# Performance work log

Hardware: AMD Instinct MI355X
Metric: run time of the kernel (lower is better)

## Reference

```python
import jax, jax.numpy as jnp
import numpy as np

NUM_BUCKETS = 32
MAX_DISTANCE = 128
NUM_HEADS = 16
D_KV = 64


def _relative_position_bucket(relative_position):
    # bidirectional buckets, faithful to T5Attention._relative_position_bucket
    num_buckets = NUM_BUCKETS // 2
    relative_buckets = (relative_position > 0).astype(jnp.int32) * num_buckets
    relative_position = jnp.abs(relative_position)
    max_exact = num_buckets // 2
    is_small = relative_position < max_exact
    rp_f = relative_position.astype(jnp.float32)
    rel_if_large = max_exact + (
        jnp.log(rp_f / max_exact) / np.log(MAX_DISTANCE / max_exact) * (num_buckets - max_exact)
    )
    rel_if_large = jnp.minimum(rel_if_large, num_buckets - 1)
    relative_buckets = relative_buckets + jnp.where(is_small, rp_f, rel_if_large).astype(jnp.int32)
    return relative_buckets


def setup_inputs() -> dict:
    key = jax.random.key(0)
    ks = jax.random.split(key, 6)
    B, S, D = 2, 2048, 1024
    inner = NUM_HEADS * D_KV  # 1024
    q_std = (inner * D_KV) ** (-0.5)
    kv_std = inner ** (-0.5)
    return {
        "hidden_states": jax.random.normal(ks[0], (B, S, D), jnp.float32),
        "attention_mask": jnp.ones((B, S), jnp.int32),
        "Wq": jax.random.normal(ks[1], (D, inner), jnp.float32) * q_std,
        "Wk": jax.random.normal(ks[2], (D, inner), jnp.float32) * kv_std,
        "Wv": jax.random.normal(ks[3], (D, inner), jnp.float32) * kv_std,
        "Wo": jax.random.normal(ks[4], (inner, D), jnp.float32) * kv_std,
        "rel_bias": jax.random.normal(ks[5], (NUM_BUCKETS, NUM_HEADS), jnp.float32),
    }


def reference(hidden_states, attention_mask, Wq, Wk, Wv, Wo, rel_bias):
    B, S, D = hidden_states.shape
    H, Dk = NUM_HEADS, D_KV

    q = (hidden_states @ Wq).reshape(B, S, H, Dk)
    k = (hidden_states @ Wk).reshape(B, S, H, Dk)
    v = (hidden_states @ Wv).reshape(B, S, H, Dk)
    q = q / jnp.sqrt(jnp.asarray(Dk, q.dtype))

    scores = jnp.einsum('bthd,bshd->bhts', q, k)  # [B,H,S,S]

    # relative position bias
    pos = jnp.arange(S, dtype=jnp.int32)
    rel_pos = pos[None, :] - pos[:, None]          # memory - context, [S,S]
    buckets = _relative_position_bucket(rel_pos)   # [S,S]
    bias = rel_bias[buckets]                       # [S,S,H]
    scores = scores + bias.transpose(2, 0, 1)[None].astype(scores.dtype)

    mask = attention_mask[:, None, None, :].astype(scores.dtype)
    scores = scores + (1.0 - mask) * jnp.finfo(scores.dtype).min

    attn = jax.nn.softmax(scores, axis=-1)
    out = jnp.einsum('bhts,bshd->bthd', attn, v).reshape(B, S, H * Dk)
    return out @ Wo
```

## Files before the change

kernel.cpp:

```cpp
#include <hip/hip_runtime.h>
#include <hip/hip_bf16.h>
#include <math.h>

typedef __attribute__((ext_vector_type(8))) short bf16x8;
typedef __attribute__((ext_vector_type(4))) short s16x4;
typedef __attribute__((ext_vector_type(4))) float f32x4;

constexpr int cB = 2, cS = 2048, cH = 16, cD = 64, cIn = 1024, cM = 1024;
constexpr float cLog2e = 1.4426950408889634f;

union BfPack { bf16x8 v; short s[8]; };
union BfPack4 { s16x4 v; short s[4]; };

__device__ __forceinline__ short f2bf(float f) {
    union { float f; unsigned u; } v; v.f = f;
    unsigned r = v.u + 0x7fffu + ((v.u >> 16) & 1u);
    return (short)(r >> 16);
}

__device__ __forceinline__ f32x4 mfma16(bf16x8 a, bf16x8 b, f32x4 c) {
    return __builtin_amdgcn_mfma_f32_16x16x32_bf16(a, b, c, 0, 0, 0);
}

__device__ __forceinline__ void async16(const short* g, short* l) {
    __builtin_amdgcn_global_load_lds(
        (const __attribute__((address_space(1))) unsigned*)(uintptr_t)g,
        (__attribute__((address_space(3))) unsigned*)(uintptr_t)l, 16, 0, 0);
}

__global__ __launch_bounds__(256) void prep_kernel(
    const float* __restrict__ hidden, short* __restrict__ hbf,
    const float* __restrict__ Wq, const float* __restrict__ Wk,
    const float* __restrict__ Wv, const float* __restrict__ Wo,
    short* __restrict__ Wt,
    const float* __restrict__ rel_bias, const int* __restrict__ mask,
    float* __restrict__ bt, float* __restrict__ maskadd) {
    const int bid = blockIdx.x;
    const int tid = threadIdx.x;
    if (bid < 2048) {
        int t = bid * 256 + tid;
        const float4* src = (const float4*)hidden;
        float4 a = src[2 * t], b = src[2 * t + 1];
        BfPack p;
        p.s[0] = f2bf(a.x); p.s[1] = f2bf(a.y); p.s[2] = f2bf(a.z); p.s[3] = f2bf(a.w);
        p.s[4] = f2bf(b.x); p.s[5] = f2bf(b.y); p.s[6] = f2bf(b.z); p.s[7] = f2bf(b.w);
        ((bf16x8*)hbf)[t] = p.v;
    } else if (bid < 3072) {
        const int b2 = bid - 2048;
        const int z = b2 >> 8, rem = b2 & 255;
        const float* W = (z == 0) ? Wq : (z == 1) ? Wk : (z == 2) ? Wv : Wo;
        const float scale = (z == 0) ? 0.125f * cLog2e : 1.0f;
        const int n0 = (rem & 15) * 64, k0 = (rem >> 4) * 64;
        __shared__ short sW[64][72];
        const int r = tid >> 2, c4 = (tid & 3) * 16;
        {
            const float* src = W + (size_t)(k0 + r) * cM + n0 + c4;
            BfPack p[2];
            #pragma unroll
            for (int q = 0; q < 2; q++) {
                float4 x = ((const float4*)src)[2 * q];
                float4 y = ((const float4*)src)[2 * q + 1];
                p[q].s[0] = f2bf(x.x * scale); p[q].s[1] = f2bf(x.y * scale);
                p[q].s[2] = f2bf(x.z * scale); p[q].s[3] = f2bf(x.w * scale);
                p[q].s[4] = f2bf(y.x * scale); p[q].s[5] = f2bf(y.y * scale);
                p[q].s[6] = f2bf(y.z * scale); p[q].s[7] = f2bf(y.w * scale);
            }
            *(bf16x8*)&sW[r][c4] = p[0].v;
            *(bf16x8*)&sW[r][c4 + 8] = p[1].v;
        }
        __syncthreads();
        const int n = tid >> 2, kc = (tid & 3) * 16;
        BfPack o0, o1;
        #pragma unroll
        for (int j = 0; j < 8; j++) o0.s[j] = sW[kc + j][n];
        #pragma unroll
        for (int j = 0; j < 8; j++) o1.s[j] = sW[kc + 8 + j][n];
        short* dst = Wt + (size_t)z * cM * cIn + (size_t)(n0 + n) * cIn + k0 + kc;
        *(bf16x8*)dst = o0.v;
        *(bf16x8*)(dst + 8) = o1.v;
    } else {
        int idx = (bid - 3072) * 256 + tid;
        if (idx < 4096) maskadd[idx] = (1.0f - (float)mask[idx]) * -3.0e38f;
        if (idx >= 4095) return;
        int delta = idx - 2047;
        int rb = (delta > 0) ? 16 : 0;
        int ar = delta < 0 ? -delta : delta;
        int bucket;
        if (ar < 8) {
            bucket = rb + ar;
        } else {
            float rl = 8.0f + logf((float)ar * 0.125f) * 2.8853900817779268f;
            rl = fminf(rl, 15.0f);
            bucket = rb + (int)rl;
        }
        #pragma unroll
        for (int h = 0; h < cH; h++)
            bt[h * 4096 + 2048 + delta] = rel_bias[bucket * cH + h] * cLog2e;
    }
}

template <bool SWAP>
__device__ __forceinline__ void gemm_core(
    const short* __restrict__ A, const short* __restrict__ Bt,
    short* smem, int m0, int c0, int tid, f32x4 (&acc)[4][4]) {
    short* sA = smem;
    short* sB = smem + 4096;
    const int w = tid >> 6, l = tid & 63;
    const int m16 = l & 15, g = l >> 4;
    const int srow = l >> 2, scol = (l & 3) * 8;
    const int mq = (w & 1) * 64, nq = (w >> 1) * 64;

    for (int k0 = 0; k0 < cIn; k0 += 32) {
        __syncthreads();
        async16(A + (size_t)(m0 + w * 16 + srow) * cIn + k0 + scol,
                sA + w * 512 + l * 8);
        async16(A + (size_t)(m0 + 64 + w * 16 + srow) * cIn + k0 + scol,
                sA + 2048 + w * 512 + l * 8);
        async16(Bt + (size_t)(c0 + w * 16 + srow) * cIn + k0 + scol,
                sB + w * 512 + l * 8);
        async16(Bt + (size_t)(c0 + 64 + w * 16 + srow) * cIn + k0 + scol,
                sB + 2048 + w * 512 + l * 8);
        __syncthreads();
        bf16x8 af[4], bf[4];
        #pragma unroll
        for (int i = 0; i < 4; i++)
            af[i] = *(const bf16x8*)(sA + (mq + i * 16 + m16) * 32 + g * 8);
        #pragma unroll
        for (int j = 0; j < 4; j++)
            bf[j] = *(const bf16x8*)(sB + (nq + j * 16 + m16) * 32 + g * 8);
        #pragma unroll
        for (int i = 0; i < 4; i++)
            #pragma unroll
            for (int j = 0; j < 4; j++)
                acc[i][j] = SWAP ? mfma16(bf[j], af[i], acc[i][j])
                                 : mfma16(af[i], bf[j], acc[i][j]);
    }
}

__global__ __launch_bounds__(256) void gemm_qkv_kernel(
    const short* __restrict__ hbf, const short* __restrict__ Wt,
    short* __restrict__ Qrm, short* __restrict__ Krm, short* __restrict__ VT) {
    const int z = blockIdx.z;
    const short* Bt = Wt + (size_t)z * cM * cIn;
    const int m0 = blockIdx.y * 128, c0 = blockIdx.x * 128;
    __shared__ short smem[128 * 132];
    const int tid = threadIdx.x, w = tid >> 6, l = tid & 63;
    const int m16 = l & 15, g = l >> 4;
    const int mq = (w & 1) * 64, nq = (w >> 1) * 64;
    f32x4 acc[4][4] = {};

    if (z <= 1) {
        gemm_core<false>(hbf, Bt, smem, m0, c0, tid, acc);
        __syncthreads();
        #pragma unroll
        for (int i = 0; i < 4; i++)
            #pragma unroll
            for (int j = 0; j < 4; j++)
                #pragma unroll
                for (int r = 0; r < 4; r++)
                    smem[(mq + i * 16 + g * 4 + r) * 132 + nq + j * 16 + m16] =
                        f2bf(acc[i][j][r]);
        __syncthreads();
        const int tr = tid >> 1, hf = (tid & 1) * 64;
        short* dst = ((z == 0) ? Qrm : Krm) + (size_t)(m0 + tr) * cM + c0 + hf;
        #pragma unroll
        for (int c = 0; c < 8; c++)
            *(bf16x8*)(dst + c * 8) = *(const bf16x8*)(smem + tr * 132 + hf + c * 8);
    } else {
        gemm_core<true>(hbf, Bt, smem, m0, c0, tid, acc);
        __syncthreads();
        #pragma unroll
        for (int i = 0; i < 4; i++) {
            const int sl = mq + i * 16 + m16;
            const int s6 = sl & 63;
            const int pcol = (sl & 64) +
                             ((s6 & 3) | ((s6 & 28) << 1) | ((s6 >> 3) & 4));
            #pragma unroll
            for (int j = 0; j < 4; j++)
                #pragma unroll
                for (int r = 0; r < 4; r++)
                    smem[(nq + j * 16 + g * 4 + r) * 132 + pcol] =
                        f2bf(acc[i][j][r]);
        }
        __syncthreads();
        const int tr = tid >> 1, hf = (tid & 1) * 64;
        const int wcol = c0 + tr;
        short* dst = VT + (((size_t)(m0 >> 11) * cH + (wcol >> 6)) * cD +
                           (wcol & 63)) * cS + (m0 & 2047) + hf;
        #pragma unroll
        for (int c = 0; c < 8; c++)
            *(bf16x8*)(dst + c * 8) = *(const bf16x8*)(smem + tr * 132 + hf + c * 8);
    }
}

__global__ __launch_bounds__(256, 2) void attn_kernel(
    const short* __restrict__ Qrm, const short* __restrict__ Krm,
    const short* __restrict__ VTK, const float* __restrict__ maskadd,
    const float* __restrict__ bias_t, short* __restrict__ ctx) {
    const int raw = blockIdx.x;
    const int xcd = raw & 7, j = raw >> 3;
    const int qi = j & 15, grp = j >> 4;
    const int bh = grp * 8 + xcd;
    const int b = bh >> 4, h = bh & 15;
    const int q0 = qi * 128;

    const short* VTp = VTK + ((size_t)b * cH + h) * cS * cD;
    const float* bh_ = bias_t + h * 4096 + 2048;
    const float* mp = maskadd + b * cS;

    const int tid = threadIdx.x;
    const int wave = tid >> 6, lane = tid & 63;
    const int m16 = lane & 15, g = lane >> 4;

    __shared__ short Kt[2][128 * 64];
    __shared__ short Vt[2][64 * 128];

    int qv[2];
    bf16x8 qf[2][2];
    #pragma unroll
    for (int qq = 0; qq < 2; qq++) {
        qv[qq] = q0 + qq * 64 + wave * 16 + m16;
        const short* qb = Qrm + (size_t)(b * cS + qv[qq]) * cM + h * cD;
        qf[qq][0] = *(const bf16x8*)(qb + g * 8);
        qf[qq][1] = *(const bf16x8*)(qb + 32 + g * 8);
    }

    f32x4 o[2][4] = {};
    f32x4 lacc[2] = {};
    BfPack ones;
    #pragma unroll
    for (int i = 0; i < 8; i++) ones.s[i] = (short)0x3F80;

    const int u8 = tid & 7, r8 = tid >> 3;
    const int u16s = tid & 15, r16 = tid >> 4;
    const short* pK = Krm + ((size_t)b * cS + r8) * cM + h * cD +
                      ((u8 ^ (r8 & 7)) << 3);
    const short* pV = VTp + (size_t)r16 * cS + ((u16s ^ (r16 & 7)) << 3);
    short* dK = (short*)Kt + tid * 8;
    short* dV = (short*)Vt + tid * 8;

    const int kx0 = ((g ^ (m16 & 7)) << 3);
    const int kx1 = (((g + 4) ^ (m16 & 7)) << 3);

    #pragma unroll
    for (int c = 0; c < 4; c++) {
        async16(pK + (size_t)(c * 32) * cM, dK + c * 2048);
        async16(pV + (size_t)(c * 16) * cS, dV + c * 2048);
    }
    __syncthreads();

    for (int kt = 0; kt < cS; kt += 128) {
        const int buf = (kt >> 7) & 1, nxt = buf ^ 1;
        if (kt + 128 < cS) {
            #pragma unroll
            for (int c = 0; c < 4; c++) {
                async16(pK + (size_t)(kt + 128 + c * 32) * cM,
                        dK + nxt * 8192 + c * 2048);
                async16(pV + (size_t)(c * 16) * cS + kt + 128,
                        dV + nxt * 8192 + c * 2048);
            }
        }
        const short* K_ = (const short*)Kt + buf * 8192;
        const short* V_ = (const short*)Vt + buf * 8192;

        #pragma unroll
        for (int h2 = 0; h2 < 2; h2++) {
            f32x4 binit[2][4];
            #pragma unroll
            for (int t4 = 0; t4 < 4; t4++) {
                const int keyb = kt + (h2 * 4 + t4) * 16 + g * 4;
                #pragma unroll
                for (int qq = 0; qq < 2; qq++)
                    #pragma unroll
                    for (int c = 0; c < 4; c++)
                        binit[qq][t4][c] = bh_[keyb + c - qv[qq]] + mp[keyb + c];
            }

            f32x4 s[2][4];
            __builtin_amdgcn_s_setprio(1);
            #pragma unroll
            for (int t4 = 0; t4 < 4; t4++) {
                const int st = h2 * 4 + t4;
                bf16x8 klo = *(const bf16x8*)(K_ + (st * 16 + m16) * 64 + kx0);
                bf16x8 khi = *(const bf16x8*)(K_ + (st * 16 + m16) * 64 + kx1);
                #pragma unroll
                for (int qq = 0; qq < 2; qq++) {
                    f32x4 z4 = {};
                    s[qq][t4] = mfma16(khi, qf[qq][1],
                                       mfma16(klo, qf[qq][0], z4));
                }
            }
            __builtin_amdgcn_s_setprio(0);

            BfPack pp[2][2];
            #pragma unroll
            for (int qq = 0; qq < 2; qq++)
                #pragma unroll
                for (int t4 = 0; t4 < 4; t4++)
                    #pragma unroll
                    for (int r = 0; r < 2; r++) {
                        float p0 = __builtin_amdgcn_exp2f(s[qq][t4][2 * r] +
                                                          binit[qq][t4][2 * r]);
                        float p1 = __builtin_amdgcn_exp2f(s[qq][t4][2 * r + 1] +
                                                          binit[qq][t4][2 * r + 1]);
                        __hip_bfloat162 h2v = __float22bfloat162_rn(float2{p0, p1});
                        short2 sp = *(short2*)&h2v;
                        pp[qq][t4 & 1].s[(t4 >> 1) * 4 + 2 * r]     = sp.x;
                        pp[qq][t4 & 1].s[(t4 >> 1) * 4 + 2 * r + 1] = sp.y;
                    }

            __builtin_amdgcn_s_setprio(1);
            #pragma unroll
            for (int qq = 0; qq < 2; qq++) {
                lacc[qq] = mfma16(ones.v, pp[qq][0].v, lacc[qq]);
                lacc[qq] = mfma16(ones.v, pp[qq][1].v, lacc[qq]);
            }
            #pragma unroll
            for (int nt = 0; nt < 4; nt++) {
                bf16x8 vlo = *(const bf16x8*)(V_ + (nt * 16 + m16) * 128 +
                                              h2 * 64 + kx0);
                bf16x8 vhi = *(const bf16x8*)(V_ + (nt * 16 + m16) * 128 +
                                              h2 * 64 + kx1);
                #pragma unroll
                for (int qq = 0; qq < 2; qq++) {
                    o[qq][nt] = mfma16(vlo, pp[qq][0].v, o[qq][nt]);
                    o[qq][nt] = mfma16(vhi, pp[qq][1].v, o[qq][nt]);
                }
            }
            __builtin_amdgcn_s_setprio(0);
        }

        __syncthreads();
    }

    #pragma unroll
    for (int qq = 0; qq < 2; qq++) {
        const float inv = 1.0f / lacc[qq][0];
        short* cb = ctx + (size_t)(b * cS + qv[qq]) * cM + h * cD;
        #pragma unroll
        for (int nt = 0; nt < 4; nt++) {
            BfPack4 pk;
            #pragma unroll
            for (int r = 0; r < 4; r++) pk.s[r] = f2bf(o[qq][nt][r] * inv);
            *(s16x4*)(cb + nt * 16 + g * 4) = pk.v;
        }
    }
}

__global__ __launch_bounds__(256) void gemm_o_kernel(
    const short* __restrict__ ctx, const short* __restrict__ WoT,
    float* __restrict__ out) {
    const int m0 = blockIdx.y * 64, c0 = blockIdx.x * 128;
    __shared__ short smem[6144];
    short* sA = smem;
    short* sB = smem + 2048;
    const int tid = threadIdx.x, w = tid >> 6, l = tid & 63;
    const int m16 = l & 15, g = l >> 4;
    const int wm = (w & 1) * 32, wn = (w >> 1) * 64;
    const int sr = tid >> 2, sc = (tid & 3) * 8;
    f32x4 acc[2][4] = {};

    for (int k0 = 0; k0 < cIn; k0 += 32) {
        __syncthreads();
        async16(ctx + (size_t)(m0 + (sr & 63)) * cIn + k0 + sc, sA + tid * 8);
        async16(WoT + (size_t)(c0 + sr) * cIn + k0 + sc, sB + tid * 8);
        async16(WoT + (size_t)(c0 + 64 + sr) * cIn + k0 + sc, sB + 2048 + tid * 8);
        __syncthreads();
        bf16x8 af[2], bf[4];
        #pragma unroll
        for (int i = 0; i < 2; i++)
            af[i] = *(const bf16x8*)(sA + (wm + i * 16 + m16) * 32 + g * 8);
        #pragma unroll
        for (int jj = 0; jj < 4; jj++)
            bf[jj] = *(const bf16x8*)(sB + (wn + jj * 16 + m16) * 32 + g * 8);
        #pragma unroll
        for (int i = 0; i < 2; i++)
            #pragma unroll
            for (int jj = 0; jj < 4; jj++)
                acc[i][jj] = mfma16(af[i], bf[jj], acc[i][jj]);
    }
    #pragma unroll
    for (int i = 0; i < 2; i++)
        #pragma unroll
        for (int jj = 0; jj < 4; jj++)
            #pragma unroll
            for (int r = 0; r < 4; r++)
                out[(size_t)(m0 + wm + i * 16 + g * 4 + r) * cM +
                    c0 + wn + jj * 16 + m16] = acc[i][jj][r];
}

extern "C" void kernel_launch(void* const* d_in, const int* in_sizes, int n_in,
                              void* d_out, int out_size, void* d_ws, size_t ws_size,
                              hipStream_t stream) {
    const float* hidden   = (const float*)d_in[0];
    const int*   mask     = (const int*)d_in[1];
    const float* Wq       = (const float*)d_in[2];
    const float* Wk       = (const float*)d_in[3];
    const float* Wv       = (const float*)d_in[4];
    const float* Wo       = (const float*)d_in[5];
    const float* rel_bias = (const float*)d_in[6];
    float* out = (float*)d_out;

    short* hbf_ctx = (short*)d_ws;
    short* Wt  = hbf_ctx + (size_t)4 * 1024 * 1024;
    short* Qrm = Wt  + (size_t)4 * 1024 * 1024;
    short* Krm = Qrm + (size_t)4 * 1024 * 1024;
    short* VT  = Krm + (size_t)4 * 1024 * 1024;
    float* bias_t  = (float*)(VT + (size_t)4 * 1024 * 1024);
    float* maskf   = bias_t + 16 * 4096;

    prep_kernel<<<3088, 256, 0, stream>>>(hidden, hbf_ctx, Wq, Wk, Wv, Wo, Wt,
                                          rel_bias, mask, bias_t, maskf);
    gemm_qkv_kernel<<<dim3(8, 32, 3), 256, 0, stream>>>(hbf_ctx, Wt, Qrm, Krm, VT);
    attn_kernel<<<512, 256, 0, stream>>>(Qrm, Krm, VT, maskf, bias_t, hbf_ctx);
    gemm_o_kernel<<<dim3(8, 64), 256, 0, stream>>>(hbf_ctx, Wt + (size_t)3 * 1024 * 1024,
                                                   out);
}
```

Measured before the change: 197.1 us.

## Load V directly from global into registers and vectorize bias loads via phase-shifted tables

The attention kernel stops staging V tiles through shared memory and instead loads V fragments straight from global memory into registers each half-tile. The relative-position bias table is expanded into four phase-shifted copies, so each lane can read its four bias values as one aligned float4; the mask add is likewise read as a float4. This cuts LDS traffic and footprint and replaces scalar gathers with vector loads, at the cost of uncached global V reads on the critical path and a four-times-larger bias table written in prep.

```diff
diff --git a/kernel.cpp b/kernel.cpp
--- a/kernel.cpp
+++ b/kernel.cpp
@@ -80,22 +80,26 @@
         *(bf16x8*)(dst + 8) = o1.v;
     } else {
         int idx = (bid - 3072) * 256 + tid;
-        if (idx < 4096) maskadd[idx] = (1.0f - (float)mask[idx]) * -3.0e38f;
-        if (idx >= 4095) return;
-        int delta = idx - 2047;
-        int rb = (delta > 0) ? 16 : 0;
-        int ar = delta < 0 ? -delta : delta;
-        int bucket;
-        if (ar < 8) {
-            bucket = rb + ar;
-        } else {
-            float rl = 8.0f + logf((float)ar * 0.125f) * 2.8853900817779268f;
-            rl = fminf(rl, 15.0f);
-            bucket = rb + (int)rl;
-        }
-        #pragma unroll
-        for (int h = 0; h < cH; h++)
-            bt[h * 4096 + 2048 + delta] = rel_bias[bucket * cH + h] * cLog2e;
+        maskadd[idx] = (1.0f - (float)mask[idx]) * -3.0e38f;
+        #pragma unroll
+        for (int p = 0; p < 4; p++) {
+            int delta = idx - 2048 + p;
+            if (delta > 2047) delta = 2047;
+            int rb = (delta > 0) ? 16 : 0;
+            int ar = delta < 0 ? -delta : delta;
+            int bucket;
+            if (ar < 8) {
+                bucket = rb + ar;
+            } else {
+                float rl = 8.0f + logf((float)ar * 0.125f) * 2.8853900817779268f;
+                rl = fminf(rl, 15.0f);
+                bucket = rb + (int)rl;
+            }
+            #pragma unroll
+            for (int h = 0; h < cH; h++)
+                bt[((size_t)(p * cH + h)) * 4096 + idx] =
+                    rel_bias[bucket * cH + h] * cLog2e;
+        }
     }
 }
 
@@ -196,7 +200,7 @@
 __global__ __launch_bounds__(256, 2) void attn_kernel(
     const short* __restrict__ Qrm, const short* __restrict__ Krm,
     const short* __restrict__ VTK, const float* __restrict__ maskadd,
-    const float* __restrict__ bias_t, short* __restrict__ ctx) {
+    const float* __restrict__ bias4, short* __restrict__ ctx) {
     const int raw = blockIdx.x;
     const int xcd = raw & 7, j = raw >> 3;
     const int qi = j & 15, grp = j >> 4;
@@ -205,7 +209,6 @@
     const int q0 = qi * 128;
 
     const short* VTp = VTK + ((size_t)b * cH + h) * cS * cD;
-    const float* bh_ = bias_t + h * 4096 + 2048;
     const float* mp = maskadd + b * cS;
 
     const int tid = threadIdx.x;
@@ -213,7 +216,6 @@
     const int m16 = lane & 15, g = lane >> 4;
 
     __shared__ short Kt[2][128 * 64];
-    __shared__ short Vt[2][64 * 128];
 
     int qv[2];
     bf16x8 qf[2][2];
@@ -225,6 +227,12 @@
         qf[qq][1] = *(const bf16x8*)(qb + 32 + g * 8);
     }
 
+    const int ph = (-(m16 & 3)) & 3;
+    const float* bq[2];
+    #pragma unroll
+    for (int qq = 0; qq < 2; qq++)
+        bq[qq] = bias4 + ((size_t)(ph * cH + h)) * 4096 + 2048 - qv[qq] - ph;
+
     f32x4 o[2][4] = {};
     f32x4 lacc[2] = {};
     BfPack ones;
@@ -232,48 +240,47 @@
     for (int i = 0; i < 8; i++) ones.s[i] = (short)0x3F80;
 
     const int u8 = tid & 7, r8 = tid >> 3;
-    const int u16s = tid & 15, r16 = tid >> 4;
     const short* pK = Krm + ((size_t)b * cS + r8) * cM + h * cD +
                       ((u8 ^ (r8 & 7)) << 3);
-    const short* pV = VTp + (size_t)r16 * cS + ((u16s ^ (r16 & 7)) << 3);
     short* dK = (short*)Kt + tid * 8;
-    short* dV = (short*)Vt + tid * 8;
 
     const int kx0 = ((g ^ (m16 & 7)) << 3);
     const int kx1 = (((g + 4) ^ (m16 & 7)) << 3);
 
     #pragma unroll
-    for (int c = 0; c < 4; c++) {
+    for (int c = 0; c < 4; c++)
         async16(pK + (size_t)(c * 32) * cM, dK + c * 2048);
-        async16(pV + (size_t)(c * 16) * cS, dV + c * 2048);
-    }
     __syncthreads();
 
     for (int kt = 0; kt < cS; kt += 128) {
         const int buf = (kt >> 7) & 1, nxt = buf ^ 1;
         if (kt + 128 < cS) {
             #pragma unroll
-            for (int c = 0; c < 4; c++) {
+            for (int c = 0; c < 4; c++)
                 async16(pK + (size_t)(kt + 128 + c * 32) * cM,
                         dK + nxt * 8192 + c * 2048);
-                async16(pV + (size_t)(c * 16) * cS + kt + 128,
-                        dV + nxt * 8192 + c * 2048);
-            }
         }
         const short* K_ = (const short*)Kt + buf * 8192;
-        const short* V_ = (const short*)Vt + buf * 8192;
 
         #pragma unroll
         for (int h2 = 0; h2 < 2; h2++) {
+            bf16x8 vf[4][2];
+            #pragma unroll
+            for (int nt = 0; nt < 4; nt++) {
+                const short* vb = VTp + (size_t)(nt * 16 + m16) * cS +
+                                  kt + h2 * 64 + g * 8;
+                vf[nt][0] = *(const bf16x8*)vb;
+                vf[nt][1] = *(const bf16x8*)(vb + 32);
+            }
+
             f32x4 binit[2][4];
             #pragma unroll
             for (int t4 = 0; t4 < 4; t4++) {
                 const int keyb = kt + (h2 * 4 + t4) * 16 + g * 4;
+                f32x4 mk = *(const f32x4*)(mp + keyb);
                 #pragma unroll
                 for (int qq = 0; qq < 2; qq++)
-                    #pragma unroll
-                    for (int c = 0; c < 4; c++)
-                        binit[qq][t4][c] = bh_[keyb + c - qv[qq]] + mp[keyb + c];
+                    binit[qq][t4] = *(const f32x4*)(bq[qq] + keyb) + mk;
             }
 
             f32x4 s[2][4];
@@ -317,14 +324,10 @@
             }
             #pragma unroll
             for (int nt = 0; nt < 4; nt++) {
-                bf16x8 vlo = *(const bf16x8*)(V_ + (nt * 16 + m16) * 128 +
-                                              h2 * 64 + kx0);
-                bf16x8 vhi = *(const bf16x8*)(V_ + (nt * 16 + m16) * 128 +
-                                              h2 * 64 + kx1);
                 #pragma unroll
                 for (int qq = 0; qq < 2; qq++) {
-                    o[qq][nt] = mfma16(vlo, pp[qq][0].v, o[qq][nt]);
-                    o[qq][nt] = mfma16(vhi, pp[qq][1].v, o[qq][nt]);
+                    o[qq][nt] = mfma16(vf[nt][0], pp[qq][0].v, o[qq][nt]);
+                    o[qq][nt] = mfma16(vf[nt][1], pp[qq][1].v, o[qq][nt]);
                 }
             }
             __builtin_amdgcn_s_setprio(0);
@@ -407,7 +410,7 @@
     short* Krm = Qrm + (size_t)4 * 1024 * 1024;
     short* VT  = Krm + (size_t)4 * 1024 * 1024;
     float* bias_t  = (float*)(VT + (size_t)4 * 1024 * 1024);
-    float* maskf   = bias_t + 16 * 4096;
+    float* maskf   = bias_t + (size_t)4 * 16 * 4096;
 
     prep_kernel<<<3088, 256, 0, stream>>>(hidden, hbf_ctx, Wq, Wk, Wv, Wo, Wt,
                                           rel_bias, mask, bias_t, maskf);
```

Result: slower. 266.9 us (+35.4%).

## Deepen GEMM K-tile to 64 with XOR-swizzled LDS layout; vectorize mask load

Applied to the files above, without the earlier changes.

The shared GEMM core now stages 64-wide K slices per iteration instead of 32, using an XOR swizzle on the 16-byte column chunk to avoid LDS bank conflicts. This halves the number of barrier pairs per K loop and doubles MFMA work between syncs. It also raises LDS use, and it depends on the smem buffer being large enough for 8192-element A and B tiles. In the attention kernel, the mask values are read once as a float4 vector instead of as scalar loads.

```diff
diff --git a/kernel.cpp b/kernel.cpp
--- a/kernel.cpp
+++ b/kernel.cpp
@@ -104,36 +104,48 @@
     const short* __restrict__ A, const short* __restrict__ Bt,
     short* smem, int m0, int c0, int tid, f32x4 (&acc)[4][4]) {
     short* sA = smem;
-    short* sB = smem + 4096;
+    short* sB = smem + 8192;
     const int w = tid >> 6, l = tid & 63;
     const int m16 = l & 15, g = l >> 4;
-    const int srow = l >> 2, scol = (l & 3) * 8;
     const int mq = (w & 1) * 64, nq = (w >> 1) * 64;
 
-    for (int k0 = 0; k0 < cIn; k0 += 32) {
-        __syncthreads();
-        async16(A + (size_t)(m0 + w * 16 + srow) * cIn + k0 + scol,
-                sA + w * 512 + l * 8);
-        async16(A + (size_t)(m0 + 64 + w * 16 + srow) * cIn + k0 + scol,
-                sA + 2048 + w * 512 + l * 8);
-        async16(Bt + (size_t)(c0 + w * 16 + srow) * cIn + k0 + scol,
-                sB + w * 512 + l * 8);
-        async16(Bt + (size_t)(c0 + 64 + w * 16 + srow) * cIn + k0 + scol,
-                sB + 2048 + w * 512 + l * 8);
-        __syncthreads();
-        bf16x8 af[4], bf[4];
+    const int u8 = tid & 7, r8 = tid >> 3;
+    const short* pA = A + (size_t)(m0 + r8) * cIn + ((u8 ^ (r8 & 7)) << 3);
+    const short* pB = Bt + (size_t)(c0 + r8) * cIn + ((u8 ^ (r8 & 7)) << 3);
+    short* dA = sA + tid * 8;
+    short* dB = sB + tid * 8;
+
+    const int kx0 = ((g ^ (m16 & 7)) << 3);
+    const int kx1 = (((g + 4) ^ (m16 & 7)) << 3);
+
+    for (int k0 = 0; k0 < cIn; k0 += 64) {
+        __syncthreads();
+        #pragma unroll
+        for (int c = 0; c < 4; c++) {
+            async16(pA + (size_t)(c * 32) * cIn + k0, dA + c * 2048);
+            async16(pB + (size_t)(c * 32) * cIn + k0, dB + c * 2048);
+        }
+        __syncthreads();
+        bf16x8 af[4][2], bf[4][2];
+        #pragma unroll
+        for (int i = 0; i < 4; i++) {
+            af[i][0] = *(const bf16x8*)(sA + (mq + i * 16 + m16) * 64 + kx0);
+            af[i][1] = *(const bf16x8*)(sA + (mq + i * 16 + m16) * 64 + kx1);
+        }
+        #pragma unroll
+        for (int j = 0; j < 4; j++) {
+            bf[j][0] = *(const bf16x8*)(sB + (nq + j * 16 + m16) * 64 + kx0);
+            bf[j][1] = *(const bf16x8*)(sB + (nq + j * 16 + m16) * 64 + kx1);
+        }
         #pragma unroll
         for (int i = 0; i < 4; i++)
-            af[i] = *(const bf16x8*)(sA + (mq + i * 16 + m16) * 32 + g * 8);
-        #pragma unroll
-        for (int j = 0; j < 4; j++)
-            bf[j] = *(const bf16x8*)(sB + (nq + j * 16 + m16) * 32 + g * 8);
-        #pragma unroll
-        for (int i = 0; i < 4; i++)
-            #pragma unroll
-            for (int j = 0; j < 4; j++)
-                acc[i][j] = SWAP ? mfma16(bf[j], af[i], acc[i][j])
-                                 : mfma16(af[i], bf[j], acc[i][j]);
+            #pragma unroll
+            for (int j = 0; j < 4; j++) {
+                acc[i][j] = SWAP ? mfma16(bf[j][0], af[i][0], acc[i][j])
+                                 : mfma16(af[i][0], bf[j][0], acc[i][j]);
+                acc[i][j] = SWAP ? mfma16(bf[j][1], af[i][1], acc[i][j])
+                                 : mfma16(af[i][1], bf[j][1], acc[i][j]);
+            }
     }
 }
 
@@ -269,11 +281,12 @@
             #pragma unroll
             for (int t4 = 0; t4 < 4; t4++) {
                 const int keyb = kt + (h2 * 4 + t4) * 16 + g * 4;
+                f32x4 mk = *(const f32x4*)(mp + keyb);
                 #pragma unroll
                 for (int qq = 0; qq < 2; qq++)
                     #pragma unroll
                     for (int c = 0; c < 4; c++)
-                        binit[qq][t4][c] = bh_[keyb + c - qv[qq]] + mp[keyb + c];
+                        binit[qq][t4][c] = bh_[keyb + c - qv[qq]] + mk[c];
             }
 
             f32x4 s[2][4];
```

Result: slower. 204.7 us (+3.8%).
